# Kernel optimization log

Hardware: AMD Instinct MI355X
Metric: run time of the kernel (lower is better)

## Reference

```python
import jax, jax.numpy as jnp
import numpy as np

# ---- left-hand kinematic constants (from ShadowHandModule.create_left_hand_nodes_and_joints) ----
N_NODES = 29
PARENTS = [-1, 0, 1, 2, 3, 4, 5, 1, 7, 8, 9, 10, 1, 12, 13, 14, 15, 1, 17, 18, 19, 20, 21, 1, 23, 24, 25, 26, 27]
# joint index driving each node (-1 = fixed link such as fingertips)
NODE_JOINT = [0, 1, 2, 3, 4, 5, -1, 6, 7, 8, 9, -1, 10, 11, 12, 13, -1, 14, 15, 16, 17, 18, -1, 19, 20, 21, 22, 23, -1]
TRANS = np.array([
    [0.0, 0.0, 0.0], [0.0, 0.0, 0.034],
    [-0.033, 0.0, 0.095], [0.0, 0.0, 0.0], [0.0, 0.0, 0.045], [0.0, 0.0, 0.025], [0.0, 0.0, 0.026],
    [-0.011, 0.0, 0.099], [0.0, 0.0, 0.0], [0.0, 0.0, 0.045], [0.0, 0.0, 0.025], [0.0, 0.0, 0.026],
    [0.011, 0.0, 0.095], [0.0, 0.0, 0.0], [0.0, 0.0, 0.045], [0.0, 0.0, 0.025], [0.0, 0.0, 0.026],
    [0.033, 0.0, 0.02071], [0.0, 0.0, 0.06579], [0.0, 0.0, 0.0], [0.0, 0.0, 0.045], [0.0, 0.0, 0.025], [0.0, 0.0, 0.026],
    [-0.034, -0.0085, 0.029], [0.0, 0.0, 0.0], [0.0, 0.0, 0.038], [0.0, 0.0, 0.0], [0.0, 0.0, 0.032], [0.0, 0.0, 0.0275],
], dtype=np.float32)
AXES = np.array([
    [0.0, 1.0, 0.0], [1.0, 0.0, 0.0],
    [0.0, 1.0, 0.0], [1.0, 0.0, 0.0], [1.0, 0.0, 0.0], [1.0, 0.0, 0.0],
    [0.0, 1.0, 0.0], [1.0, 0.0, 0.0], [1.0, 0.0, 0.0], [1.0, 0.0, 0.0],
    [0.0, -1.0, 0.0], [1.0, 0.0, 0.0], [1.0, 0.0, 0.0], [1.0, 0.0, 0.0],
    [0.573576, 0.0, -0.819152], [0.0, -1.0, 0.0], [1.0, 0.0, 0.0], [1.0, 0.0, 0.0], [1.0, 0.0, 0.0],
    [0.0, 0.0, 1.0], [-1.0, 0.0, 0.0], [1.0, 0.0, 0.0], [0.0, -1.0, 0.0], [1.0, 0.0, 0.0],
], dtype=np.float32)
MIN_RAD = np.array([-0.523599, -0.698132, -0.349066, 0.0, 0.0, 0.0, -0.349066, 0.0, 0.0, 0.0,
                    -0.349066, 0.0, 0.0, 0.0, 0.0, -0.349066, 0.0, 0.0, 0.0,
                    -1.0472, 0.0, -0.20944, -0.698132, 0.0], dtype=np.float32)
MAX_RAD = np.array([0.174533, 0.488692, 0.349066, 1.5708, 1.5708, 1.5708, 0.349066, 1.5708, 1.5708, 1.5708,
                    0.349066, 1.5708, 1.5708, 1.5708, 0.785398, 0.349066, 1.5708, 1.5708, 1.5708,
                    1.0472, 1.22173, 0.20944, 0.698132, 1.5708], dtype=np.float32)
THBASE_QUAT = np.array([0.0, 0.382683, 0.0, -0.92388], dtype=np.float32)
THDISTAL_QUAT = np.array([0.707107, 0.0, 0.0, -0.707107], dtype=np.float32)
BATCH = 262144


def hat(v):
    x, y, z = v[..., 0], v[..., 1], v[..., 2]
    o = jnp.zeros_like(x)
    return jnp.stack([jnp.stack([o, -z, y], -1),
                      jnp.stack([z, o, -x], -1),
                      jnp.stack([-y, x, o], -1)], -2)


def rot_angle_axis(angle, axis):
    # angle [B,J], axis [J,3] -> [B,J,3,3] (Rodrigues)
    s = jnp.sin(angle)[..., None, None]
    c = jnp.cos(angle)[..., None, None]
    K = hat(axis)          # [J,3,3]
    K2 = jnp.matmul(K, K)  # [J,3,3]
    return jnp.eye(3, dtype=angle.dtype) + s * K + (1.0 - c) * K2


def rot_from_quat(q):
    w, x, y, z = q[0], q[1], q[2], q[3]
    return jnp.array([
        [1.0 - 2.0 * (y * y + z * z), 2.0 * (x * y - z * w), 2.0 * (x * z + y * w)],
        [2.0 * (x * y + z * w), 1.0 - 2.0 * (x * x + z * z), 2.0 * (y * z - x * w)],
        [2.0 * (x * z - y * w), 2.0 * (y * z + x * w), 1.0 - 2.0 * (x * x + y * y)],
    ], dtype=q.dtype)


def setup_inputs() -> dict:
    key = jax.random.key(0)
    u = jax.random.uniform(key, (BATCH, 24), dtype=jnp.float32)
    angles = jnp.asarray(MIN_RAD) + u * jnp.asarray(MAX_RAD - MIN_RAD)
    return {"angles": angles}


def reference(angles):
    # angles: [B, 24] joint angles -> node positions [B, 29, 3]
    B = angles.shape[0]
    q = jnp.clip(angles, jnp.asarray(MIN_RAD), jnp.asarray(MAX_RAD))
    Rj = rot_angle_axis(q, jnp.asarray(AXES))  # [B,24,3,3]
    fixed = {23: rot_from_quat(jnp.asarray(THBASE_QUAT)),
             27: rot_from_quat(jnp.asarray(THDISTAL_QUAT))}
    eye = jnp.broadcast_to(jnp.eye(3, dtype=angles.dtype), (B, 3, 3))
    Rg = [None] * N_NODES
    tg = [None] * N_NODES
    for i in range(N_NODES):  # fixed 29-node kinematic tree, topological order
        j = NODE_JOINT[i]
        Rl = Rj[:, j] if j >= 0 else eye
        if i in fixed:  # body quat applied before joint rotation (MJCF convention)
            Rl = jnp.einsum('ij,bjk->bik', fixed[i], Rl)
        tl = jnp.asarray(TRANS[i])
        p = PARENTS[i]
        if p < 0:
            Rg[i] = Rl
            tg[i] = jnp.broadcast_to(tl, (B, 3))
        else:
            # multiply_transform: (Rp @ Rl, Rp @ tl + tp)
            Rg[i] = jnp.einsum('bij,bjk->bik', Rg[p], Rl)
            tg[i] = jnp.einsum('bij,j->bi', Rg[p], tl) + tg[p]
    return jnp.stack(tg, axis=1)  # [B, 29, 3]
```

## Files before the change

kernel.cpp:

```cpp
#include <hip/hip_runtime.h>

namespace fk {

typedef float f32x4 __attribute__((ext_vector_type(4)));

struct V3 { float x, y, z; };
struct M3 { V3 c0, c1, c2; };

__device__ __forceinline__ V3 axpy(float a, V3 x, V3 y) {
    return V3{ fmaf(a, x.x, y.x), fmaf(a, x.y, y.y), fmaf(a, x.z, y.z) };
}
__device__ __forceinline__ V3 sc(float a, V3 x) { return V3{ a * x.x, a * x.y, a * x.z }; }

__device__ __forceinline__ M3 mulRx(const M3& R, float s, float c) {
    return M3{ R.c0,
               axpy(s,  R.c2, sc(c, R.c1)),
               axpy(-s, R.c1, sc(c, R.c2)) };
}
__device__ __forceinline__ M3 mulRy(const M3& R, float s, float c) {
    return M3{ axpy(-s, R.c2, sc(c, R.c0)),
               R.c1,
               axpy(s,  R.c0, sc(c, R.c2)) };
}

__device__ __forceinline__ void load_angles(f32x4 v[6], const float* __restrict__ angles,
                                            long long elem, int B) {
    if (elem < B) {
        const f32x4* ap = reinterpret_cast<const f32x4*>(angles + (size_t)elem * 24);
        #pragma unroll
        for (int m = 0; m < 6; ++m) v[m] = ap[m];
    }
}

__device__ __forceinline__ void compute_element(const f32x4 v[6], float* o) {
    float q[24];
    #pragma unroll
    for (int m = 0; m < 6; ++m) {
        q[m*4+0] = v[m].x; q[m*4+1] = v[m].y; q[m*4+2] = v[m].z; q[m*4+3] = v[m].w;
    }

    constexpr float MN[24] = {-0.523599f,-0.698132f,-0.349066f,0.f,0.f,0.f,-0.349066f,0.f,0.f,0.f,
                              -0.349066f,0.f,0.f,0.f,0.f,-0.349066f,0.f,0.f,0.f,
                              -1.0472f,0.f,-0.20944f,-0.698132f,0.f};
    constexpr float MX[24] = {0.174533f,0.488692f,0.349066f,1.5708f,1.5708f,1.5708f,0.349066f,1.5708f,1.5708f,1.5708f,
                              0.349066f,1.5708f,1.5708f,1.5708f,0.785398f,0.349066f,1.5708f,1.5708f,1.5708f,
                              1.0472f,1.22173f,0.20944f,0.698132f,1.5708f};
    float s[24], c[24];
    #pragma unroll
    for (int j = 0; j < 24; ++j) {
        float a = fminf(fmaxf(q[j], MN[j]), MX[j]);
        __sincosf(a, &s[j], &c[j]);
    }

    auto emit = [&](int node, V3 t) {
        o[node*3+0] = t.x; o[node*3+1] = t.y; o[node*3+2] = t.z;
    };

    M3 R0{ V3{c[0],0.f,-s[0]}, V3{0.f,1.f,0.f}, V3{s[0],0.f,c[0]} };
    emit(0, V3{0.f,0.f,0.f});
    M3 R1 = mulRx(R0, s[1], c[1]);
    V3 t1 = sc(0.034f, R0.c2);
    emit(1, t1);

    auto finger = [&](int n0, float sy, float cy,
                      float s1, float c1, float s2, float c2, float s3, float c3,
                      float bx, float bz) {
        M3 Ra = mulRy(R1, sy, cy);
        V3 ta = axpy(bx, R1.c0, axpy(bz, R1.c2, t1));
        emit(n0, ta);
        M3 Rb = mulRx(Ra, s1, c1);
        emit(n0+1, ta);
        V3 tc = axpy(0.045f, Rb.c2, ta);
        M3 Rc = mulRx(Rb, s2, c2);
        emit(n0+2, tc);
        V3 td = axpy(0.025f, Rc.c2, tc);
        M3 Rd = mulRx(Rc, s3, c3);
        emit(n0+3, td);
        emit(n0+4, axpy(0.026f, Rd.c2, td));
    };
    finger(2,   s[2],  c[2],  s[3],c[3],   s[4],c[4],   s[5],c[5],  -0.033f, 0.095f);
    finger(7,   s[6],  c[6],  s[7],c[7],   s[8],c[8],   s[9],c[9],  -0.011f, 0.099f);
    finger(12, -s[10], c[10], s[11],c[11], s[12],c[12], s[13],c[13], 0.011f, 0.095f);

    {
        const float ux = 0.573576f, uz = -0.819152f;
        float omc = 1.f - c[14];
        float l00 = fmaf(omc * ux, ux, c[14]);
        float l10 = s[14] * uz;
        float l20 = omc * ux * uz;
        float l01 = -s[14] * uz;
        float l21 = s[14] * ux;
        float l02 = omc * ux * uz;
        float l12 = -s[14] * ux;
        float l22 = fmaf(omc * uz, uz, c[14]);
        M3 R17;
        R17.c0 = axpy(l20, R1.c2, axpy(l10,  R1.c1, sc(l00, R1.c0)));
        R17.c1 = axpy(l21, R1.c2, axpy(c[14],R1.c1, sc(l01, R1.c0)));
        R17.c2 = axpy(l22, R1.c2, axpy(l12,  R1.c1, sc(l02, R1.c0)));
        V3 t17 = axpy(0.033f, R1.c0, axpy(0.02071f, R1.c2, t1));
        emit(17, t17);
        V3 t18 = axpy(0.06579f, R17.c2, t17);
        M3 R18 = mulRy(R17, -s[15], c[15]);
        emit(18, t18);
        M3 R19 = mulRx(R18, s[16], c[16]);
        emit(19, t18);
        V3 t20 = axpy(0.045f, R19.c2, t18);
        M3 R20 = mulRx(R19, s[17], c[17]);
        emit(20, t20);
        V3 t21 = axpy(0.025f, R20.c2, t20);
        M3 R21 = mulRx(R20, s[18], c[18]);
        emit(21, t21);
        emit(22, axpy(0.026f, R21.c2, t21));
    }

    {
        const float k = 0.70710678f;
        float m00 = -k * c[19], m10 = -s[19];
        float m01 =  k * s[19], m11 = -c[19];
        M3 R23;
        R23.c0 = axpy(m00, R1.c2, axpy(m10, R1.c1, sc(m00, R1.c0)));
        R23.c1 = axpy(m01, R1.c2, axpy(m11, R1.c1, sc(m01, R1.c0)));
        R23.c2 = axpy(k, R1.c2, sc(-k, R1.c0));
        V3 t23 = axpy(-0.034f, R1.c0, axpy(-0.0085f, R1.c1, axpy(0.029f, R1.c2, t1)));
        emit(23, t23);
        M3 R24 = mulRx(R23, -s[20], c[20]);
        emit(24, t23);
        V3 t25 = axpy(0.038f, R24.c2, t23);
        M3 R25 = mulRx(R24, s[21], c[21]);
        emit(25, t25);
        M3 R26 = mulRy(R25, -s[22], c[22]);
        emit(26, t25);
        V3 t27 = axpy(0.032f, R26.c2, t25);
        M3 R27;
        R27.c0 = sc(-1.f, R26.c1);
        R27.c1 = axpy(s[23],  R26.c2, sc(c[23], R26.c0));
        R27.c2 = axpy(-s[23], R26.c0, sc(c[23], R26.c2));
        emit(27, t27);
        emit(28, axpy(0.0275f, R27.c2, t27));
    }
}

__device__ __forceinline__ void flush_slab(const float* lds, float* __restrict__ out,
                                           long long s, int tid, int B) {
    const size_t base_f = (size_t)s * 64 * 87;
    if ((s + 1) * 64 <= (long long)B) {
        const f32x4* lsrc = reinterpret_cast<const f32x4*>(lds);
        f32x4* gdst = reinterpret_cast<f32x4*>(out + base_f);
        #pragma unroll
        for (int m = 0; m < 21; ++m)
            __builtin_nontemporal_store(lsrc[m * 64 + tid], &gdst[m * 64 + tid]);
        int g = 21 * 64 + tid;
        if (g < 1392) __builtin_nontemporal_store(lsrc[g], &gdst[g]);
    } else {
        const size_t limit = (size_t)B * 87;
        for (int m = 0; m < 87; ++m) {
            size_t f = (size_t)m * 64 + tid;
            if (base_f + f < limit) __builtin_nontemporal_store(lds[f], &out[base_f + f]);
        }
    }
}

__global__ __launch_bounds__(64) void fk_kernel(const float* __restrict__ angles,
                                                float* __restrict__ out,
                                                int B, int S, int K) {
    __shared__ float lds[64 * 87];
    const int tid = threadIdx.x;

    long long s = (long long)blockIdx.x * K;
    if (s >= S) return;
    const long long s_end = min((long long)S, s + K);

    f32x4 a6[6];
    load_angles(a6, angles, s * 64 + tid, B);

    for (; s < s_end; ++s) {
        compute_element(a6, lds + tid * 87);
        if (s + 1 < s_end)
            load_angles(a6, angles, (s + 1) * 64 + tid, B);
        flush_slab(lds, out, s, tid, B);
    }
}

}

extern "C" void kernel_launch(void* const* d_in, const int* in_sizes, int n_in,
                              void* d_out, int out_size, void* d_ws, size_t ws_size,
                              hipStream_t stream) {
    const float* angles = (const float*)d_in[0];
    float* out = (float*)d_out;
    const int B = in_sizes[0] / 24;
    const int S = (B + 63) / 64;
    const int grid = S < 1024 ? S : 1024;
    const int K = (S + grid - 1) / grid;
    fk::fk_kernel<<<grid, 64, 0, stream>>>(angles, out, B, S, K);
}
```

Measured before the change: 24.25 us.

## Launch one block per slab and stage output through half-sized LDS

```diff
diff --git a/kernel.cpp b/kernel.cpp
--- a/kernel.cpp
+++ b/kernel.cpp
@@ -140,44 +140,52 @@
     }
 }
 
-__device__ __forceinline__ void flush_slab(const float* lds, float* __restrict__ out,
-                                           long long s, int tid, int B) {
-    const size_t base_f = (size_t)s * 64 * 87;
-    if ((s + 1) * 64 <= (long long)B) {
-        const f32x4* lsrc = reinterpret_cast<const f32x4*>(lds);
-        f32x4* gdst = reinterpret_cast<f32x4*>(out + base_f);
-        #pragma unroll
-        for (int m = 0; m < 21; ++m)
-            __builtin_nontemporal_store(lsrc[m * 64 + tid], &gdst[m * 64 + tid]);
-        int g = 21 * 64 + tid;
-        if (g < 1392) __builtin_nontemporal_store(lsrc[g], &gdst[g]);
-    } else {
-        const size_t limit = (size_t)B * 87;
-        for (int m = 0; m < 87; ++m) {
-            size_t f = (size_t)m * 64 + tid;
-            if (base_f + f < limit) __builtin_nontemporal_store(lds[f], &out[base_f + f]);
-        }
-    }
-}
-
-__global__ __launch_bounds__(64) void fk_kernel(const float* __restrict__ angles,
-                                                float* __restrict__ out,
-                                                int B, int S, int K) {
-    __shared__ float lds[64 * 87];
+__device__ __forceinline__ void flush_half(const float* lds, float* __restrict__ gout,
+                                           int tid) {
+    const f32x4* lsrc = reinterpret_cast<const f32x4*>(lds);
+    f32x4* gdst = reinterpret_cast<f32x4*>(gout);
+    #pragma unroll
+    for (int m = 0; m < 10; ++m)
+        __builtin_nontemporal_store(lsrc[m * 64 + tid], &gdst[m * 64 + tid]);
+    if (tid < 56) __builtin_nontemporal_store(lsrc[640 + tid], &gdst[640 + tid]);
+}
+
+__device__ __forceinline__ void flush_half_guarded(const float* lds, float* __restrict__ out,
+                                                   long long e0, int tid, int B) {
+    const size_t limit = (size_t)B * 87;
+    const size_t base = (size_t)e0 * 87;
+    for (int m = 0; m < 44; ++m) {
+        int f = m * 64 + tid;
+        if (f < 2784 && base + f < limit)
+            __builtin_nontemporal_store(lds[f], &out[base + f]);
+    }
+}
+
+__global__ __launch_bounds__(64, 3) void fk_kernel(const float* __restrict__ angles,
+                                                   float* __restrict__ out, int B) {
+    __shared__ float lds[32 * 87];
     const int tid = threadIdx.x;
-
-    long long s = (long long)blockIdx.x * K;
-    if (s >= S) return;
-    const long long s_end = min((long long)S, s + K);
+    const long long s = blockIdx.x;
+    const long long e = s * 64 + tid;
 
     f32x4 a6[6];
-    load_angles(a6, angles, s * 64 + tid, B);
-
-    for (; s < s_end; ++s) {
-        compute_element(a6, lds + tid * 87);
-        if (s + 1 < s_end)
-            load_angles(a6, angles, (s + 1) * 64 + tid, B);
-        flush_slab(lds, out, s, tid, B);
+    load_angles(a6, angles, e, B);
+
+    if (tid < 32 && e < B) compute_element(a6, lds + tid * 87);
+    __syncthreads();
+    if (s * 64 + 32 <= (long long)B)
+        flush_half(lds, out + (size_t)s * 64 * 87, tid);
+    else
+        flush_half_guarded(lds, out, s * 64, tid, B);
+    __syncthreads();
+
+    if (tid >= 32 && e < B) compute_element(a6, lds + (tid - 32) * 87);
+    __syncthreads();
+    if (s * 64 + 32 < (long long)B) {
+        if (s * 64 + 64 <= (long long)B)
+            flush_half(lds, out + ((size_t)s * 64 + 32) * 87, tid);
+        else
+            flush_half_guarded(lds, out, s * 64 + 32, tid, B);
     }
 }
 
@@ -189,8 +197,6 @@
     const float* angles = (const float*)d_in[0];
     float* out = (float*)d_out;
     const int B = in_sizes[0] / 24;
-    const int S = (B + 63) / 64;
-    const int grid = S < 1024 ? S : 1024;
-    const int K = (S + grid - 1) / grid;
-    fk::fk_kernel<<<grid, 64, 0, stream>>>(angles, out, B, S, K);
-}
+    const int grid = (B + 63) / 64;
+    fk::fk_kernel<<<grid, 64, 0, stream>>>(angles, out, B);
+}
```

After: 25.52 us. +5.2%, slower.
